# Kernel optimization log

Measured on AMD Instinct MI355X. Metric: run time of the kernel, lower is better.

The kernel has to match this reference:

```python
import jax, jax.numpy as jnp
import numpy as np

D_MODEL = 512
NUM_HEADS = 8
HEAD_DIM = D_MODEL // NUM_HEADS
WINDOW = 64


def setup_inputs() -> dict:
    key = jax.random.key(0)
    ks = jax.random.split(key, 9)
    B, S = 2, 4096
    s = 1.0 / np.sqrt(D_MODEL)
    x = jax.random.normal(ks[0], (B, S, D_MODEL), dtype=jnp.float32)
    Wq = jax.random.uniform(ks[1], (D_MODEL, D_MODEL), jnp.float32, -s, s)
    bq = jax.random.uniform(ks[2], (D_MODEL,), jnp.float32, -s, s)
    Wk = jax.random.uniform(ks[3], (D_MODEL, D_MODEL), jnp.float32, -s, s)
    bk = jax.random.uniform(ks[4], (D_MODEL,), jnp.float32, -s, s)
    Wv = jax.random.uniform(ks[5], (D_MODEL, D_MODEL), jnp.float32, -s, s)
    bv = jax.random.uniform(ks[6], (D_MODEL,), jnp.float32, -s, s)
    Wo = jax.random.uniform(ks[7], (D_MODEL, D_MODEL), jnp.float32, -s, s)
    bo = jax.random.uniform(ks[8], (D_MODEL,), jnp.float32, -s, s)
    return {"x": x, "Wq": Wq, "bq": bq, "Wk": Wk, "bk": bk,
            "Wv": Wv, "bv": bv, "Wo": Wo, "bo": bo}


def reference(x, Wq, bq, Wk, bk, Wv, bv, Wo, bo):
    B, S, _ = x.shape
    # projections (torch Linear: x @ W.T + b)
    q = (x @ Wq.T + bq).reshape(B, S, NUM_HEADS, HEAD_DIM).transpose(0, 2, 1, 3)
    k = (x @ Wk.T + bk).reshape(B, S, NUM_HEADS, HEAD_DIM).transpose(0, 2, 1, 3)
    v = (x @ Wv.T + bv).reshape(B, S, NUM_HEADS, HEAD_DIM).transpose(0, 2, 1, 3)
    scores = jnp.einsum('bhqd,bhkd->bhqk', q, k) / jnp.sqrt(
        jnp.asarray(HEAD_DIM, x.dtype))
    idx = jnp.arange(S)
    local = jnp.abs(idx[None, :] - idx[:, None]) <= WINDOW  # [S,S]
    scores = jnp.where(local[None, None], scores, -jnp.inf)
    attn = jax.nn.softmax(scores, axis=-1)
    out = jnp.einsum('bhqk,bhkd->bhqd', attn, v)
    out = out.transpose(0, 2, 1, 3).reshape(B, S, D_MODEL)
    return out @ Wo.T + bo
```

## Files before the change

### kernel.cpp

```cpp
#include <hip/hip_runtime.h>
#include <hip/hip_bf16.h>

typedef __attribute__((ext_vector_type(8))) short short8;
typedef __attribute__((ext_vector_type(4))) float f32x4;

#define S_LEN 4096
#define DM 512
#define NH 8
#define HD 64
#define NB 2

__device__ __forceinline__ ushort f2bf(float f) {
    union { float f; unsigned int i; } x; x.f = f;
    unsigned int i = x.i;
    unsigned int r = (i + 0x7fffu + ((i >> 16) & 1u)) >> 16;
    return (ushort)r;
}

__device__ __forceinline__ void gload16(const ushort* g, ushort* l) {
    __builtin_amdgcn_global_load_lds(
        (const __attribute__((address_space(1))) unsigned int*)(g),
        (__attribute__((address_space(3))) unsigned int*)(l),
        16, 0, 0);
}

__global__ __launch_bounds__(256) void cvt_all_kernel(
    const float* __restrict__ x,
    const float* __restrict__ s0, const float* __restrict__ s1,
    const float* __restrict__ s2, const float* __restrict__ s3,
    ushort* __restrict__ xb,
    ushort* __restrict__ t0, ushort* __restrict__ t1,
    ushort* __restrict__ t2, ushort* __restrict__ t3)
{
    const float* src;
    ushort* dst;
    size_t i;
    if (blockIdx.x < 2048) {
        src = x; dst = xb;
        i = (size_t)blockIdx.x * 256 + threadIdx.x;
    } else {
        const int wb = blockIdx.x - 2048;
        const int which = wb >> 7;
        src = (which == 0) ? s0 : (which == 1) ? s1 : (which == 2) ? s2 : s3;
        dst = (which == 0) ? t0 : (which == 1) ? t1 : (which == 2) ? t2 : t3;
        i = (size_t)(wb & 127) * 256 + threadIdx.x;
    }
    const float4* s = (const float4*)src;
    float4 a = s[i * 2], b = s[i * 2 + 1];
    short8 o;
    o[0] = (short)f2bf(a.x); o[1] = (short)f2bf(a.y);
    o[2] = (short)f2bf(a.z); o[3] = (short)f2bf(a.w);
    o[4] = (short)f2bf(b.x); o[5] = (short)f2bf(b.y);
    o[6] = (short)f2bf(b.z); o[7] = (short)f2bf(b.w);
    *(short8*)(dst + i * 8) = o;
}

__global__ __launch_bounds__(256) void qkv_proj_kernel(
    const ushort* __restrict__ X,
    const ushort* __restrict__ Wq, const float* __restrict__ bq,
    const ushort* __restrict__ Wk, const float* __restrict__ bk,
    const ushort* __restrict__ Wv, const float* __restrict__ bv,
    ushort* __restrict__ Qws, ushort* __restrict__ Kws, ushort* __restrict__ Vt)
{
    __shared__ __align__(1024) ushort As[128 * 64];
    __shared__ __align__(1024) ushort Bs[128 * 64];

    const int lane = threadIdx.x & 63;
    const int w    = threadIdx.x >> 6;
    const int xcd  = blockIdx.x & 7;
    const int idx  = blockIdx.x >> 3;
    const int tr   = xcd + 8 * (idx / 12);
    const int tc   = idx % 12;
    const int which = tc >> 2;
    const int c0   = (tc & 3) * 128;
    const int r0   = tr * 128;

    const ushort* W    = (which == 0) ? Wq : (which == 1) ? Wk : Wv;
    const float*  bias = (which == 0) ? bq : (which == 1) ? bk : bv;

    const int lr = lane & 15;
    const int lg = lane >> 4;
    const int wr = w >> 1, wc = w & 1;
    const int ldrow = lane >> 3;
    const int ldcol = (lane & 7) * 8;

    f32x4 acc[4][4] = {};
    for (int ks = 0; ks < 8; ks++) {
        const int k0 = ks * 64;
        if (ks) __syncthreads();
        const ushort* gA = X + (size_t)(r0 + ldrow) * DM + k0 + ldcol;
        const ushort* gB = W + (size_t)(c0 + ldrow) * DM + k0 + ldcol;
#pragma unroll
        for (int j = 0; j < 4; j++) {
            const int ch = w * 4 + j;
            gload16(gA + (size_t)ch * 8 * DM, As + ch * 512);
            gload16(gB + (size_t)ch * 8 * DM, Bs + ch * 512);
        }
        __syncthreads();

#pragma unroll
        for (int kk = 0; kk < 2; kk++) {
            const int koff = kk * 32 + lg * 8;
            short8 a[4], b[4];
#pragma unroll
            for (int m = 0; m < 4; m++)
                a[m] = *(const short8*)(As + (wr * 64 + 16 * m + lr) * 64 + koff);
#pragma unroll
            for (int n = 0; n < 4; n++)
                b[n] = *(const short8*)(Bs + (wc * 64 + 16 * n + lr) * 64 + koff);
#pragma unroll
            for (int m = 0; m < 4; m++)
#pragma unroll
                for (int n = 0; n < 4; n++)
                    acc[m][n] = __builtin_amdgcn_mfma_f32_16x16x32_bf16(a[m], b[n], acc[m][n], 0, 0, 0);
        }
    }

#pragma unroll
    for (int n = 0; n < 4; n++) {
        const int c = c0 + wc * 64 + 16 * n + lr;
        const float bb = bias[c];
        const int h = c >> 6, d = c & 63;
#pragma unroll
        for (int m = 0; m < 4; m++) {
#pragma unroll
            for (int r = 0; r < 4; r++) {
                const int row = r0 + wr * 64 + 16 * m + 4 * lg + r;
                const int bidx = row >> 12;
                const int s = row & (S_LEN - 1);
                const ushort o = f2bf(acc[m][n][r] + bb);
                if (which == 2) {
                    Vt[((size_t)(bidx * NH + h) * HD + d) * S_LEN + s] = o;
                } else {
                    ushort* dst = (which == 0) ? Qws : Kws;
                    dst[((size_t)(bidx * NH + h) * S_LEN + s) * HD + d] = o;
                }
            }
        }
    }
}

__global__ __launch_bounds__(256) void attn_kernel(
    const ushort* __restrict__ Qws, const ushort* __restrict__ Kws,
    const ushort* __restrict__ Vt, ushort* __restrict__ AO)
{
    __shared__ __align__(1024) ushort Ks[192 * 64];
    __shared__ __align__(1024) ushort Vs[64 * 192];
    __shared__ ushort Pl[4][16][200];

    const int x   = blockIdx.x;
    const int xcd = x & 7;
    const int idx = x >> 3;
    const int bh  = xcd * 2 + (idx >> 6);
    const int qb  = idx & 63;
    const int w   = threadIdx.x >> 6;
    const int lane = threadIdx.x & 63;
    const int lr = lane & 15;
    const int lg = lane >> 4;

    const ushort* Qh = Qws + (size_t)bh * S_LEN * HD;
    const ushort* Kh = Kws + (size_t)bh * S_LEN * HD;
    const ushort* Vh = Vt  + (size_t)bh * HD * S_LEN;

    const int q0 = qb * 64 + w * 16;
    const int kstart = qb * 64 - 64;

#pragma unroll
    for (int i = 0; i < 6; i++) {
        const int sb = w * 384 + i * 64;
        const int s = sb + lane;
        const int row = s >> 3;
        const int g = (s & 7) ^ (row & 7);
        int rg = kstart + row;
        rg = (rg < 0) ? 0 : (rg >= S_LEN ? S_LEN - 1 : rg);
        gload16(Kh + (size_t)rg * HD + g * 8, Ks + sb * 8);
    }
#pragma unroll
    for (int i = 0; i < 6; i++) {
        const int sb = w * 384 + i * 64;
        const int s = sb + lane;
        const int row = s / 24;
        const int sr = s - row * 24;
        const int cr = sr ^ (row & 7);
        int cg = kstart + cr * 8;
        cg = (cg < 0) ? 0 : (cg > S_LEN - 8 ? S_LEN - 8 : cg);
        gload16(Vh + (size_t)row * S_LEN + cg, Vs + sb * 8);
    }

    short8 qa[2];
#pragma unroll
    for (int kk = 0; kk < 2; kk++)
        qa[kk] = *(const short8*)(Qh + (size_t)(q0 + lr) * HD + kk * 32 + lg * 8);

    __syncthreads();

    const int swz = (lr & 7) << 3;

    f32x4 sc[12];
#pragma unroll
    for (int ct = 0; ct < 12; ct++) {
        sc[ct] = f32x4{0.f, 0.f, 0.f, 0.f};
        const int kr = ct * 16 + lr;
        const int base = kr * 64;
        short8 kb0 = *(const short8*)(Ks + (base + ((0  + lg * 8) ^ swz)));
        short8 kb1 = *(const short8*)(Ks + (base + ((32 + lg * 8) ^ swz)));
        sc[ct] = __builtin_amdgcn_mfma_f32_16x16x32_bf16(qa[0], kb0, sc[ct], 0, 0, 0);
        sc[ct] = __builtin_amdgcn_mfma_f32_16x16x32_bf16(qa[1], kb1, sc[ct], 0, 0, 0);
    }

    const float scale2 = 0.18033688f;
    float inv4[4];
#pragma unroll
    for (int r = 0; r < 4; r++) {
        const int i = q0 + 4 * lg + r;
        float sum = 0.f;
#pragma unroll
        for (int ct = 0; ct < 12; ct++) {
            const int j = kstart + ct * 16 + lr;
            const bool valid = (j >= 0) && (j < S_LEN) && (i - j <= 64) && (j - i <= 64);
            const float p = valid ? exp2f(sc[ct][r] * scale2) : 0.f;
            sc[ct][r] = p;
            sum += p;
        }
        sum += __shfl_xor(sum, 1);
        sum += __shfl_xor(sum, 2);
        sum += __shfl_xor(sum, 4);
        sum += __shfl_xor(sum, 8);
        inv4[r] = 1.0f / sum;
    }

#pragma unroll
    for (int ct = 0; ct < 12; ct++)
#pragma unroll
        for (int r = 0; r < 4; r++)
            Pl[w][4 * lg + r][ct * 16 + lr] = f2bf(sc[ct][r]);

    f32x4 po[4] = {};
#pragma unroll
    for (int kk2 = 0; kk2 < 6; kk2++) {
        short8 pa = *(const short8*)(&Pl[w][lr][kk2 * 32 + lg * 8]);
#pragma unroll
        for (int n = 0; n < 4; n++) {
            const int vbase = (16 * n + lr) * 192;
            short8 vv = *(const short8*)(Vs + (vbase + ((kk2 * 32 + lg * 8) ^ swz)));
            po[n] = __builtin_amdgcn_mfma_f32_16x16x32_bf16(pa, vv, po[n], 0, 0, 0);
        }
    }

    const int b = bh >> 3, h = bh & 7;
#pragma unroll
    for (int n = 0; n < 4; n++) {
#pragma unroll
        for (int r = 0; r < 4; r++) {
            const int srow = q0 + 4 * lg + r;
            AO[((size_t)(b * S_LEN + srow)) * DM + h * HD + n * 16 + lr] =
                f2bf(po[n][r] * inv4[r]);
        }
    }
}

__global__ __launch_bounds__(256) void out_proj_kernel(
    const ushort* __restrict__ AO, const ushort* __restrict__ Wo,
    const float* __restrict__ bo, float* __restrict__ Out)
{
    __shared__ __align__(1024) ushort As[128 * 64];
    __shared__ __align__(1024) ushort Bs[128 * 64];

    const int lane = threadIdx.x & 63;
    const int w    = threadIdx.x >> 6;
    const int xcd  = blockIdx.x & 7;
    const int idx  = blockIdx.x >> 3;
    const int tr   = xcd + 8 * (idx >> 2);
    const int tc   = idx & 3;
    const int c0   = tc * 128;
    const int r0   = tr * 128;
    const int lr = lane & 15;
    const int lg = lane >> 4;
    const int wr = w >> 1, wc = w & 1;
    const int ldrow = lane >> 3;
    const int ldcol = (lane & 7) * 8;

    f32x4 acc[4][4] = {};
    for (int ks = 0; ks < 8; ks++) {
        const int k0 = ks * 64;
        if (ks) __syncthreads();
        const ushort* gA = AO + (size_t)(r0 + ldrow) * DM + k0 + ldcol;
        const ushort* gB = Wo + (size_t)(c0 + ldrow) * DM + k0 + ldcol;
#pragma unroll
        for (int j = 0; j < 4; j++) {
            const int ch = w * 4 + j;
            gload16(gA + (size_t)ch * 8 * DM, As + ch * 512);
            gload16(gB + (size_t)ch * 8 * DM, Bs + ch * 512);
        }
        __syncthreads();

#pragma unroll
        for (int kk = 0; kk < 2; kk++) {
            const int koff = kk * 32 + lg * 8;
            short8 a[4], b[4];
#pragma unroll
            for (int m = 0; m < 4; m++)
                a[m] = *(const short8*)(As + (wr * 64 + 16 * m + lr) * 64 + koff);
#pragma unroll
            for (int n = 0; n < 4; n++)
                b[n] = *(const short8*)(Bs + (wc * 64 + 16 * n + lr) * 64 + koff);
#pragma unroll
            for (int m = 0; m < 4; m++)
#pragma unroll
                for (int n = 0; n < 4; n++)
                    acc[m][n] = __builtin_amdgcn_mfma_f32_16x16x32_bf16(a[m], b[n], acc[m][n], 0, 0, 0);
        }
    }

#pragma unroll
    for (int n = 0; n < 4; n++) {
        const int c = c0 + wc * 64 + 16 * n + lr;
        const float bb = bo[c];
#pragma unroll
        for (int m = 0; m < 4; m++) {
#pragma unroll
            for (int r = 0; r < 4; r++) {
                const int row = r0 + wr * 64 + 16 * m + 4 * lg + r;
                Out[(size_t)row * DM + c] = acc[m][n][r] + bb;
            }
        }
    }
}

extern "C" void kernel_launch(void* const* d_in, const int* in_sizes, int n_in,
                              void* d_out, int out_size, void* d_ws, size_t ws_size,
                              hipStream_t stream) {
    const float* x  = (const float*)d_in[0];
    const float* Wq = (const float*)d_in[1];
    const float* bq = (const float*)d_in[2];
    const float* Wk = (const float*)d_in[3];
    const float* bk = (const float*)d_in[4];
    const float* Wv = (const float*)d_in[5];
    const float* bv = (const float*)d_in[6];
    const float* Wo = (const float*)d_in[7];
    const float* bo = (const float*)d_in[8];
    float* out = (float*)d_out;

    const size_t XE = (size_t)NB * S_LEN * DM;
    const size_t WE = (size_t)DM * DM;

    ushort* Xb  = (ushort*)d_ws;
    ushort* Wqb = Xb + XE;
    ushort* Wkb = Wqb + WE;
    ushort* Wvb = Wkb + WE;
    ushort* Wob = Wvb + WE;
    ushort* Qws = Wob + WE;
    ushort* Kws = Qws + XE;
    ushort* Vt  = Kws + XE;
    ushort* AO  = Vt + XE;

    cvt_all_kernel<<<2560, 256, 0, stream>>>(x, Wq, Wk, Wv, Wo, Xb, Wqb, Wkb, Wvb, Wob);
    qkv_proj_kernel<<<768, 256, 0, stream>>>(Xb, Wqb, bq, Wkb, bk, Wvb, bv, Qws, Kws, Vt);
    attn_kernel<<<1024, 256, 0, stream>>>(Qws, Kws, Vt, AO);
    out_proj_kernel<<<256, 256, 0, stream>>>(AO, Wob, bo, out);
}
```

Before: 65.42 us.

## Keep attention probabilities in registers by transposing QK^T MFMA operands

The score MFMA now takes K as operand A and Q as operand B, so each lane holds a column of scores for one query. The probabilities can then feed the PV MFMA directly as the B operand through 16x16x16 bf16 MFMAs, which removes the LDS staging buffer and its write, sync and read. The row-sum reduction shrinks to two cross-group shuffles, and the output is written as packed 8-byte stores per lane. In exchange it issues twice as many smaller PV MFMAs and does 4-element LDS reads of V.

```diff
diff --git a/kernel.cpp b/kernel.cpp
--- a/kernel.cpp
+++ b/kernel.cpp
@@ -2,6 +2,7 @@
 #include <hip/hip_bf16.h>
 
 typedef __attribute__((ext_vector_type(8))) short short8;
+typedef __attribute__((ext_vector_type(4))) short s16x4;
 typedef __attribute__((ext_vector_type(4))) float f32x4;
 
 #define S_LEN 4096
@@ -22,6 +23,17 @@
         (const __attribute__((address_space(1))) unsigned int*)(g),
         (__attribute__((address_space(3))) unsigned int*)(l),
         16, 0, 0);
+}
+
+__device__ __forceinline__ f32x4 mfma16(s16x4 a, s16x4 b, f32x4 c) {
+#if __has_builtin(__builtin_amdgcn_mfma_f32_16x16x16bf16_1k)
+    return __builtin_amdgcn_mfma_f32_16x16x16bf16_1k(a, b, c, 0, 0, 0);
+#else
+    f32x4 d;
+    asm volatile("v_mfma_f32_16x16x16_bf16 %0, %1, %2, %3"
+                 : "=v"(d) : "v"(a), "v"(b), "v"(c));
+    return d;
+#endif
 }
 
 __global__ __launch_bounds__(256) void cvt_all_kernel(
@@ -146,7 +158,6 @@
 {
     __shared__ __align__(1024) ushort Ks[192 * 64];
     __shared__ __align__(1024) ushort Vs[64 * 192];
-    __shared__ ushort Pl[4][16][200];
 
     const int x   = blockIdx.x;
     const int xcd = x & 7;
@@ -200,62 +211,62 @@
 #pragma unroll
     for (int ct = 0; ct < 12; ct++) {
         sc[ct] = f32x4{0.f, 0.f, 0.f, 0.f};
-        const int kr = ct * 16 + lr;
-        const int base = kr * 64;
+        const int base = (ct * 16 + lr) * 64;
         short8 kb0 = *(const short8*)(Ks + (base + ((0  + lg * 8) ^ swz)));
         short8 kb1 = *(const short8*)(Ks + (base + ((32 + lg * 8) ^ swz)));
-        sc[ct] = __builtin_amdgcn_mfma_f32_16x16x32_bf16(qa[0], kb0, sc[ct], 0, 0, 0);
-        sc[ct] = __builtin_amdgcn_mfma_f32_16x16x32_bf16(qa[1], kb1, sc[ct], 0, 0, 0);
+        sc[ct] = __builtin_amdgcn_mfma_f32_16x16x32_bf16(kb0, qa[0], sc[ct], 0, 0, 0);
+        sc[ct] = __builtin_amdgcn_mfma_f32_16x16x32_bf16(kb1, qa[1], sc[ct], 0, 0, 0);
     }
 
     const float scale2 = 0.18033688f;
-    float inv4[4];
-#pragma unroll
-    for (int r = 0; r < 4; r++) {
-        const int i = q0 + 4 * lg + r;
-        float sum = 0.f;
-#pragma unroll
-        for (int ct = 0; ct < 12; ct++) {
-            const int j = kstart + ct * 16 + lr;
-            const bool valid = (j >= 0) && (j < S_LEN) && (i - j <= 64) && (j - i <= 64);
+    const int qi = q0 + lr;
+    float sum = 0.f;
+#pragma unroll
+    for (int ct = 0; ct < 12; ct++) {
+#pragma unroll
+        for (int r = 0; r < 4; r++) {
+            const int j = kstart + ct * 16 + 4 * lg + r;
+            const bool valid = (j >= 0) && (j < S_LEN) && (qi - j <= 64) && (j - qi <= 64);
             const float p = valid ? exp2f(sc[ct][r] * scale2) : 0.f;
             sc[ct][r] = p;
             sum += p;
         }
-        sum += __shfl_xor(sum, 1);
-        sum += __shfl_xor(sum, 2);
-        sum += __shfl_xor(sum, 4);
-        sum += __shfl_xor(sum, 8);
-        inv4[r] = 1.0f / sum;
-    }
-
-#pragma unroll
-    for (int ct = 0; ct < 12; ct++)
-#pragma unroll
-        for (int r = 0; r < 4; r++)
-            Pl[w][4 * lg + r][ct * 16 + lr] = f2bf(sc[ct][r]);
+    }
+    sum += __shfl_xor(sum, 16);
+    sum += __shfl_xor(sum, 32);
+    const float inv = 1.0f / sum;
+
+    s16x4 pb[12];
+#pragma unroll
+    for (int ct = 0; ct < 12; ct++) {
+        pb[ct][0] = (short)f2bf(sc[ct][0]);
+        pb[ct][1] = (short)f2bf(sc[ct][1]);
+        pb[ct][2] = (short)f2bf(sc[ct][2]);
+        pb[ct][3] = (short)f2bf(sc[ct][3]);
+    }
 
     f32x4 po[4] = {};
 #pragma unroll
-    for (int kk2 = 0; kk2 < 6; kk2++) {
-        short8 pa = *(const short8*)(&Pl[w][lr][kk2 * 32 + lg * 8]);
+    for (int ct = 0; ct < 12; ct++) {
+        const int k0 = ct * 16 + 4 * lg;
+        const int sub = k0 & 7;
+        const int ch = k0 >> 3;
 #pragma unroll
         for (int n = 0; n < 4; n++) {
-            const int vbase = (16 * n + lr) * 192;
-            short8 vv = *(const short8*)(Vs + (vbase + ((kk2 * 32 + lg * 8) ^ swz)));
-            po[n] = __builtin_amdgcn_mfma_f32_16x16x32_bf16(pa, vv, po[n], 0, 0, 0);
+            const int d = 16 * n + lr;
+            s16x4 va = *(const s16x4*)(Vs + d * 192 + 8 * (ch ^ (lr & 7)) + sub);
+            po[n] = mfma16(va, pb[ct], po[n]);
         }
     }
 
     const int b = bh >> 3, h = bh & 7;
+    ushort* aorow = AO + ((size_t)(b * S_LEN + q0 + lr)) * DM + h * HD;
 #pragma unroll
     for (int n = 0; n < 4; n++) {
-#pragma unroll
-        for (int r = 0; r < 4; r++) {
-            const int srow = q0 + 4 * lg + r;
-            AO[((size_t)(b * S_LEN + srow)) * DM + h * HD + n * 16 + lr] =
-                f2bf(po[n][r] * inv4[r]);
-        }
+        uint2 u;
+        u.x = (uint)f2bf(po[n][0] * inv) | ((uint)f2bf(po[n][1] * inv) << 16);
+        u.y = (uint)f2bf(po[n][2] * inv) | ((uint)f2bf(po[n][3] * inv) << 16);
+        *(uint2*)(aorow + 16 * n + 4 * lg) = u;
     }
 }
 
```

Measured after the change: 65.16 us. No clear change (-0.4%).
